# Kernel tuning notes

Hardware: AMD Instinct MI355X
Metric: run time of the kernel (lower is better)

The kernel has to match this reference:

```python
import jax, jax.numpy as jnp
import numpy as np

NUM_EMB = 16384
EMB_DIM = 64
BETA = 0.25  # commitment_cost, legacy=True formulation


def _l2norm(x, axis=-1):
    # matches F.normalize(p=2): x / max(||x||, 1e-12)
    n = jnp.sqrt(jnp.sum(x * x, axis=axis, keepdims=True))
    return x / jnp.maximum(n, 1e-12)


def setup_inputs() -> dict:
    key = jax.random.key(0)
    k_z, k_cb, k_w, k_b = jax.random.split(key, 4)
    z = jax.random.normal(k_z, (16, 1024, EMB_DIM), dtype=jnp.float32)
    # frozen codebook: N(0, d^{-0.5})
    codebook = jax.random.normal(k_cb, (NUM_EMB, EMB_DIM), dtype=jnp.float32) * (EMB_DIM ** -0.5)
    # Linear(d, d) default init: U(-1/sqrt(d), 1/sqrt(d))
    lim = 1.0 / np.sqrt(EMB_DIM)
    proj_w = jax.random.uniform(k_w, (EMB_DIM, EMB_DIM), dtype=jnp.float32, minval=-lim, maxval=lim)
    proj_b = jax.random.uniform(k_b, (EMB_DIM,), dtype=jnp.float32, minval=-lim, maxval=lim)
    scale = jnp.float32(10.0)  # l2_norm_scale
    return {"z": z, "codebook": codebook, "proj_w": proj_w, "proj_b": proj_b, "scale": scale}


def reference(z, codebook, proj_w, proj_b, scale):
    B, T, d = z.shape
    zf = z.reshape(-1, d)                                   # [BT, d]
    quant_codebook = codebook @ proj_w.T + proj_b           # [N, d]
    zn = _l2norm(zf)
    cn = _l2norm(quant_codebook)
    distances = -jnp.einsum('bd,nd->bn', zn, cn) * scale    # [BT, N]
    idx = jnp.argmin(distances, axis=1)                     # [BT]
    quantized = quant_codebook[idx].reshape(z.shape)        # [B, T, d]
    sg = jax.lax.stop_gradient
    commitment_loss = jnp.mean((sg(quantized) - z) ** 2)
    codebook_loss = jnp.mean((quantized - sg(z)) ** 2)
    vq_loss = commitment_loss + BETA * codebook_loss        # legacy=True
    quantized_st = z + sg(quantized - z)                    # straight-through
    return quantized_st, vq_loss, idx.reshape(B, T)
```

## Files before the change

kernel.cpp:

```cpp
#include <hip/hip_runtime.h>
#include <hip/hip_bf16.h>


#define NCODES 16384
#define NTOK   16384
#define DIM    64
#define MARGIN_MFMA 8e-3f
#define CAP    16

typedef __attribute__((ext_vector_type(8))) short bf16x8;
typedef __attribute__((ext_vector_type(4))) float f32x4;
#define GLOBAL_AS __attribute__((address_space(1)))
#define LDS_AS    __attribute__((address_space(3)))

__device__ float  g_qcb[NCODES * DIM];
__device__ short  g_cnb[NCODES * DIM];
__device__ short  g_znb[NTOK * DIM];
__device__ unsigned g_topu[NTOK];
__device__ int    g_candcnt[NTOK];
__device__ int    g_cand[NTOK * CAP];
__device__ int    g_wl[NTOK];
__device__ int    g_wln;
__device__ float  g_partial[512];

__device__ __forceinline__ float wave_sum64(float v) {
#pragma unroll
  for (int o = 32; o > 0; o >>= 1) v += __shfl_xor(v, o, 64);
  return v;
}
__device__ __forceinline__ short f2bf(float f) {
  __hip_bfloat16 h = __float2bfloat16(f);
  return *reinterpret_cast<short*>(&h);
}
__device__ __forceinline__ float bf2f(short s) {
  __hip_bfloat16 h = *reinterpret_cast<__hip_bfloat16*>(&s);
  return __bfloat162float(h);
}
__device__ __forceinline__ void split8(const float* v, bf16x8& hi, bf16x8& lo) {
#pragma unroll
  for (int i = 0; i < 8; ++i) {
    float f = v[i];
    short h = f2bf(f);
    hi[i] = h;
    lo[i] = f2bf(f - bf2f(h));
  }
}

__global__ __launch_bounds__(256) void k_prep(const float* __restrict__ cb,
                                              const float* __restrict__ pw,
                                              const float* __restrict__ pb,
                                              const float* __restrict__ z) {
  int tid = threadIdx.x;
  int wave = tid >> 6, lane = tid & 63, quad = lane >> 4, col = lane & 15;
  if (blockIdx.x < 256) {
    int rowBase = blockIdx.x * 64 + wave * 16;
    const float* cr = cb + (size_t)(rowBase + col) * 64 + quad * 8;
    bf16x8 ah0, al0, ah1, al1;
    split8(cr, ah0, al0);
    split8(cr + 32, ah1, al1);
    float vals[4][4];
    float nr[4] = {0.f, 0.f, 0.f, 0.f};
    const f32x4 fz = {0.f, 0.f, 0.f, 0.f};
#pragma unroll
    for (int nt = 0; nt < 4; ++nt) {
      int j = col + 16 * nt;
      const float* wr = pw + (size_t)j * 64 + quad * 8;
      bf16x8 bh0, bl0, bh1, bl1;
      split8(wr, bh0, bl0);
      split8(wr + 32, bh1, bl1);
      f32x4 d = __builtin_amdgcn_mfma_f32_16x16x32_bf16(ah0, bh0, fz, 0, 0, 0);
      d = __builtin_amdgcn_mfma_f32_16x16x32_bf16(ah1, bh1, d, 0, 0, 0);
      d = __builtin_amdgcn_mfma_f32_16x16x32_bf16(ah0, bl0, d, 0, 0, 0);
      d = __builtin_amdgcn_mfma_f32_16x16x32_bf16(ah1, bl1, d, 0, 0, 0);
      d = __builtin_amdgcn_mfma_f32_16x16x32_bf16(al0, bh0, d, 0, 0, 0);
      d = __builtin_amdgcn_mfma_f32_16x16x32_bf16(al1, bh1, d, 0, 0, 0);
      float bj = pb[j];
#pragma unroll
      for (int r = 0; r < 4; ++r) {
        float v = d[r] + bj;
        vals[nt][r] = v;
        nr[r] = fmaf(v, v, nr[r]);
      }
    }
#pragma unroll
    for (int r = 0; r < 4; ++r) {
      float v = nr[r];
      v += __shfl_xor(v, 1, 64);
      v += __shfl_xor(v, 2, 64);
      v += __shfl_xor(v, 4, 64);
      v += __shfl_xor(v, 8, 64);
      nr[r] = 1.0f / fmaxf(sqrtf(v), 1e-12f);
    }
#pragma unroll
    for (int nt = 0; nt < 4; ++nt)
#pragma unroll
      for (int r = 0; r < 4; ++r) {
        int row = rowBase + quad * 4 + r;
        int j = col + 16 * nt;
        g_qcb[(size_t)row * 64 + j] = vals[nt][r];
        g_cnb[(size_t)row * 64 + j] = f2bf(vals[nt][r] * nr[r]);
      }
  } else {
    int zb = blockIdx.x - 256;
    int gid = zb * 256 + tid;
    if (gid < NTOK) { g_topu[gid] = 0u; g_candcnt[gid] = 0; }
    if (gid == 0) g_wln = 0;
    int base = zb * 64;
    for (int r = 0; r < 16; ++r) {
      int row = base + wave * 16 + r;
      float v = z[(size_t)row * 64 + lane];
      float tot = wave_sum64(v * v);
      g_znb[(size_t)row * 64 + lane] = f2bf(v / fmaxf(sqrtf(tot), 1e-12f));
    }
  }
}

__global__ __launch_bounds__(256) void k_mfma1() {
  __shared__ __align__(16) short smB[2][8192];
  int tid = threadIdx.x;
  int wave = tid >> 6, lane = tid & 63;
  int quad = lane >> 4, col = lane & 15;
  int tokGroup = blockIdx.x >> 4, split = blockIdx.x & 15;
  int tokBase = tokGroup * 256 + wave * 64;

  const short* za = g_znb + (size_t)(tokBase + col) * 64 + quad * 8;
  bf16x8 A0[4], A1[4];
#pragma unroll
  for (int f = 0; f < 4; ++f) {
    A0[f] = *(const bf16x8*)(za + f * 16 * 64);
    A1[f] = *(const bf16x8*)(za + f * 16 * 64 + 32);
  }
  float m[4][4];
#pragma unroll
  for (int f = 0; f < 4; ++f)
#pragma unroll
    for (int r = 0; r < 4; ++r) m[f][r] = -3.0e38f;

  const char* gsplit = (const char*)(g_cnb + (size_t)split * 1024 * 64);
  int x = col & 7;
  int s0off = ((quad ^ x) << 3);
  int s1off = (((4 | quad) ^ x) << 3);
  int goff[4];
#pragma unroll
  for (int i = 0; i < 4; ++i) {
    int cidx = wave * 256 + i * 64 + lane;
    int row = cidx >> 3, sw = cidx & 7;
    goff[i] = row * 128 + ((sw ^ (row & 7)) << 4);
  }

#pragma unroll
  for (int i = 0; i < 4; ++i)
    __builtin_amdgcn_global_load_lds((const GLOBAL_AS void*)(gsplit + goff[i]),
                                     (LDS_AS void*)(&smB[0][wave * 2048 + i * 512]), 16, 0, 0);
  __syncthreads();

  int p = 0;
  for (int s = 0; s < 8; ++s) {
    if (s < 7) {
      const char* gb = gsplit + (size_t)(s + 1) * 16384;
#pragma unroll
      for (int i = 0; i < 4; ++i)
        __builtin_amdgcn_global_load_lds((const GLOBAL_AS void*)(gb + goff[i]),
                                         (LDS_AS void*)(&smB[p ^ 1][wave * 2048 + i * 512]),
                                         16, 0, 0);
    }
    const short* bufp = smB[p];
#pragma unroll
    for (int h = 0; h < 2; ++h) {
      bf16x8 B0[4], B1[4];
#pragma unroll
      for (int t = 0; t < 4; ++t) {
        const short* lb = bufp + ((h * 4 + t) * 16 + col) * 64;
        B0[t] = *(const bf16x8*)(lb + s0off);
        B1[t] = *(const bf16x8*)(lb + s1off);
      }
#pragma unroll
      for (int t = 0; t < 4; ++t) {
#pragma unroll
        for (int f = 0; f < 4; ++f) {
          f32x4 acc = {0.f, 0.f, 0.f, 0.f};
          acc = __builtin_amdgcn_mfma_f32_16x16x32_bf16(A0[f], B0[t], acc, 0, 0, 0);
          acc = __builtin_amdgcn_mfma_f32_16x16x32_bf16(A1[f], B1[t], acc, 0, 0, 0);
#pragma unroll
          for (int r = 0; r < 4; ++r) m[f][r] = fmaxf(m[f][r], acc[r]);
        }
      }
    }
    __syncthreads();
    p ^= 1;
  }

#pragma unroll
  for (int f = 0; f < 4; ++f)
#pragma unroll
    for (int r = 0; r < 4; ++r) {
      float v = m[f][r];
      v = fmaxf(v, __shfl_xor(v, 1, 64));
      v = fmaxf(v, __shfl_xor(v, 2, 64));
      v = fmaxf(v, __shfl_xor(v, 4, 64));
      v = fmaxf(v, __shfl_xor(v, 8, 64));
      if (col == 0) {
        unsigned b = __float_as_uint(v);
        unsigned e = (b & 0x80000000u) ? ~b : (b | 0x80000000u);
        atomicMax(&g_topu[tokBase + f * 16 + quad * 4 + r], e);
      }
    }
}

__global__ __launch_bounds__(256) void k_mfma2() {
  __shared__ __align__(16) short smB[2][8192];
  int tid = threadIdx.x;
  int wave = tid >> 6, lane = tid & 63;
  int quad = lane >> 4, col = lane & 15;
  int tokGroup = blockIdx.x >> 4, split = blockIdx.x & 15;
  int tokBase = tokGroup * 256 + wave * 64;

  const short* za = g_znb + (size_t)(tokBase + col) * 64 + quad * 8;
  bf16x8 A0[4], A1[4];
#pragma unroll
  for (int f = 0; f < 4; ++f) {
    A0[f] = *(const bf16x8*)(za + f * 16 * 64);
    A1[f] = *(const bf16x8*)(za + f * 16 * 64 + 32);
  }
  float th[4][4];
#pragma unroll
  for (int f = 0; f < 4; ++f)
#pragma unroll
    for (int r = 0; r < 4; ++r) {
      unsigned u = g_topu[tokBase + f * 16 + quad * 4 + r];
      unsigned b = (u & 0x80000000u) ? (u & 0x7FFFFFFFu) : ~u;
      th[f][r] = __uint_as_float(b) - MARGIN_MFMA;
    }

  const char* gsplit = (const char*)(g_cnb + (size_t)split * 1024 * 64);
  int x = col & 7;
  int s0off = ((quad ^ x) << 3);
  int s1off = (((4 | quad) ^ x) << 3);
  int goff[4];
#pragma unroll
  for (int i = 0; i < 4; ++i) {
    int cidx = wave * 256 + i * 64 + lane;
    int row = cidx >> 3, sw = cidx & 7;
    goff[i] = row * 128 + ((sw ^ (row & 7)) << 4);
  }

#pragma unroll
  for (int i = 0; i < 4; ++i)
    __builtin_amdgcn_global_load_lds((const GLOBAL_AS void*)(gsplit + goff[i]),
                                     (LDS_AS void*)(&smB[0][wave * 2048 + i * 512]), 16, 0, 0);
  __syncthreads();

  int codeB = split * 1024 + col;
  int p = 0;
  for (int s = 0; s < 8; ++s) {
    if (s < 7) {
      const char* gb = gsplit + (size_t)(s + 1) * 16384;
#pragma unroll
      for (int i = 0; i < 4; ++i)
        __builtin_amdgcn_global_load_lds((const GLOBAL_AS void*)(gb + goff[i]),
                                         (LDS_AS void*)(&smB[p ^ 1][wave * 2048 + i * 512]),
                                         16, 0, 0);
    }
    const short* bufp = smB[p];
#pragma unroll
    for (int h = 0; h < 2; ++h) {
      bf16x8 B0[4], B1[4];
#pragma unroll
      for (int t = 0; t < 4; ++t) {
        const short* lb = bufp + ((h * 4 + t) * 16 + col) * 64;
        B0[t] = *(const bf16x8*)(lb + s0off);
        B1[t] = *(const bf16x8*)(lb + s1off);
      }
#pragma unroll
      for (int t = 0; t < 4; ++t) {
        int code = codeB + s * 128 + (h * 4 + t) * 16;
#pragma unroll
        for (int f = 0; f < 4; ++f) {
          f32x4 acc = {0.f, 0.f, 0.f, 0.f};
          acc = __builtin_amdgcn_mfma_f32_16x16x32_bf16(A0[f], B0[t], acc, 0, 0, 0);
          acc = __builtin_amdgcn_mfma_f32_16x16x32_bf16(A1[f], B1[t], acc, 0, 0, 0);
          float dmax = fmaxf(fmaxf(acc[0] - th[f][0], acc[1] - th[f][1]),
                             fmaxf(acc[2] - th[f][2], acc[3] - th[f][3]));
          if (dmax >= 0.f) {
#pragma unroll
            for (int r = 0; r < 4; ++r) {
              if (acc[r] >= th[f][r]) {
                int tok = tokBase + f * 16 + quad * 4 + r;
                int pos = atomicAdd(&g_candcnt[tok], 1);
                if (pos < CAP) g_cand[tok * CAP + pos] = code;
              }
            }
          }
        }
      }
    }
    __syncthreads();
    p ^= 1;
  }
}

__global__ __launch_bounds__(256) void k_scan() {
  __shared__ int flags[256];
  __shared__ int sbase;
  int tid = threadIdx.x;
  int tok = blockIdx.x * 256 + tid;
  int flag = (g_candcnt[tok] >= 2) ? 1 : 0;
  flags[tid] = flag;
  __syncthreads();
  if (tid == 0) {
    int run = 0;
    for (int i = 0; i < 256; ++i) {
      int f = flags[i];
      flags[i] = run;
      run += f;
    }
    sbase = atomicAdd(&g_wln, run);
  }
  __syncthreads();
  if (flag) g_wl[sbase + flags[tid]] = tok;
}

__global__ __launch_bounds__(256) void k_arb(const float* __restrict__ z,
                                             const float* __restrict__ cb,
                                             const float* __restrict__ pw,
                                             const float* __restrict__ pb) {
  __shared__ double WT[64 * 65];
  __shared__ float cbl[4][64];
  int tid = threadIdx.x;
  int wave = tid >> 6, lane = tid & 63;
  for (int e = tid; e < 4096; e += 256) {
    int j = e >> 6, k = e & 63;
    WT[k * 65 + j] = (double)pw[e];
  }
  __syncthreads();

  int wln = g_wln;
  double bj = (double)pb[lane];
  int gwave = blockIdx.x * 4 + wave;

  for (int e = gwave; e < wln; e += 4096) {
    int tok = g_wl[e];
    int cnt = g_candcnt[tok];
    double zj = (double)z[(size_t)tok * 64 + lane];
    double best = -1.0e300;
    int bi = 0x7FFFFFFF;
    int lim = (cnt <= CAP) ? cnt : 0;
    for (int c = 0; c < lim; ++c) {
      int code = g_cand[tok * CAP + c];
      cbl[wave][lane] = cb[(size_t)code * 64 + lane];
      double s0 = 0.0, s1 = 0.0, s2 = 0.0, s3 = 0.0;
#pragma unroll
      for (int kk = 0; kk < 16; ++kk) {
        s0 = fma(WT[kk * 65 + lane], (double)cbl[wave][kk], s0);
        s1 = fma(WT[(kk + 16) * 65 + lane], (double)cbl[wave][kk + 16], s1);
        s2 = fma(WT[(kk + 32) * 65 + lane], (double)cbl[wave][kk + 32], s2);
        s3 = fma(WT[(kk + 48) * 65 + lane], (double)cbl[wave][kk + 48], s3);
      }
      double qc = ((s0 + s1) + (s2 + s3)) + bj;
      double s = zj * qc, n2 = qc * qc;
#pragma unroll
      for (int o = 32; o > 0; o >>= 1) {
        s += __shfl_xor(s, o, 64);
        n2 += __shfl_xor(n2, o, 64);
      }
      double key = s / fmax(sqrt(n2), 1e-12);
      if (key > best || (key == best && code < bi)) { best = key; bi = code; }
    }
    if (cnt > CAP) {
      for (int code = 0; code < NCODES; ++code) {
        cbl[wave][lane] = cb[(size_t)code * 64 + lane];
        double s0 = 0.0, s1 = 0.0, s2 = 0.0, s3 = 0.0;
#pragma unroll
        for (int kk = 0; kk < 16; ++kk) {
          s0 = fma(WT[kk * 65 + lane], (double)cbl[wave][kk], s0);
          s1 = fma(WT[(kk + 16) * 65 + lane], (double)cbl[wave][kk + 16], s1);
          s2 = fma(WT[(kk + 32) * 65 + lane], (double)cbl[wave][kk + 32], s2);
          s3 = fma(WT[(kk + 48) * 65 + lane], (double)cbl[wave][kk + 48], s3);
        }
        double qc = ((s0 + s1) + (s2 + s3)) + bj;
        double s = zj * qc, n2 = qc * qc;
#pragma unroll
        for (int o = 32; o > 0; o >>= 1) {
          s += __shfl_xor(s, o, 64);
          n2 += __shfl_xor(n2, o, 64);
        }
        double key = s / fmax(sqrt(n2), 1e-12);
        if (key > best || (key == best && code < bi)) { best = key; bi = code; }
      }
    }
    if (lane == 0) g_cand[tok * CAP] = bi;
  }
}

__global__ __launch_bounds__(256) void k_out(const float* __restrict__ z,
                                             float* __restrict__ out0,
                                             float* __restrict__ out2) {
  __shared__ float ws[4];
  int tid = threadIdx.x;
  int wave = tid >> 6, lane = tid & 63;
  int base = blockIdx.x * 32;
  float lsum = 0.f;
  for (int r = 0; r < 8; ++r) {
    int tok = base + wave * 8 + r;
    int idx = g_cand[tok * CAP];
    float q = g_qcb[(size_t)idx * 64 + lane];
    float zv = z[(size_t)tok * 64 + lane];
    float d = q - zv;
    out0[(size_t)tok * 64 + lane] = zv + d;
    lsum = fmaf(d, d, lsum);
    if (lane == 0) out2[tok] = (float)idx;
  }
  float tot = wave_sum64(lsum);
  if (lane == 0) ws[wave] = tot;
  __syncthreads();
  if (tid == 0) g_partial[blockIdx.x] = ((ws[0] + ws[1]) + (ws[2] + ws[3]));
}

__global__ void k_loss(float* __restrict__ out1) {
  int lane = threadIdx.x;
  float s = 0.f;
#pragma unroll
  for (int i = 0; i < 8; ++i) s += g_partial[lane + 64 * i];
  s = wave_sum64(s);
  if (lane == 0) out1[0] = 1.25f * s / 1048576.0f;
}

extern "C" void kernel_launch(void* const* d_in, const int* in_sizes, int n_in,
                              void* d_out, int out_size, void* d_ws, size_t ws_size,
                              hipStream_t stream) {
  const float* z = (const float*)d_in[0];
  const float* cb = (const float*)d_in[1];
  const float* pw = (const float*)d_in[2];
  const float* pb = (const float*)d_in[3];

  float* out0 = (float*)d_out;
  float* out1 = out0 + (size_t)NTOK * DIM;
  float* out2 = out1 + 1;

  hipLaunchKernelGGL(k_prep, dim3(512), dim3(256), 0, stream, cb, pw, pb, z);
  hipLaunchKernelGGL(k_mfma1, dim3(1024), dim3(256), 0, stream);
  hipLaunchKernelGGL(k_mfma2, dim3(1024), dim3(256), 0, stream);
  hipLaunchKernelGGL(k_scan, dim3(64), dim3(256), 0, stream);
  hipLaunchKernelGGL(k_arb, dim3(1024), dim3(256), 0, stream, z, cb, pw, pb);
  hipLaunchKernelGGL(k_out, dim3(512), dim3(256), 0, stream, z, out0, out2);
  hipLaunchKernelGGL(k_loss, dim3(1), dim3(64), 0, stream, out1);
}
```

Baseline: 194.2 us.

## Fuse scan, arbitration, output and loss kernels into one final kernel

Replaces the worklist scan, the fp64 arbitration kernel, the output kernel and the single-block loss kernel with one kernel. Each wave arbitrates its own ambiguous tokens in place and then writes the outputs. The loss is reduced by the last block to finish, found through an atomic counter with release/acquire ordering. This removes three launches and the worklist round trip. The cost is that arbitration work is no longer load-balanced across waves and each block must stage the fp64 weight matrix in LDS, with only 512 blocks instead of 1024.

```diff
diff --git a/kernel.cpp b/kernel.cpp
--- a/kernel.cpp
+++ b/kernel.cpp
@@ -19,8 +19,7 @@
 __device__ unsigned g_topu[NTOK];
 __device__ int    g_candcnt[NTOK];
 __device__ int    g_cand[NTOK * CAP];
-__device__ int    g_wl[NTOK];
-__device__ int    g_wln;
+__device__ int    g_done;
 __device__ float  g_partial[512];
 
 __device__ __forceinline__ float wave_sum64(float v) {
@@ -104,7 +103,7 @@
     int zb = blockIdx.x - 256;
     int gid = zb * 256 + tid;
     if (gid < NTOK) { g_topu[gid] = 0u; g_candcnt[gid] = 0; }
-    if (gid == 0) g_wln = 0;
+    if (gid == 0) g_done = 0;
     int base = zb * 64;
     for (int r = 0; r < 16; ++r) {
       int row = base + wave * 16 + r;
@@ -299,33 +298,17 @@
   }
 }
 
-__global__ __launch_bounds__(256) void k_scan() {
-  __shared__ int flags[256];
-  __shared__ int sbase;
-  int tid = threadIdx.x;
-  int tok = blockIdx.x * 256 + tid;
-  int flag = (g_candcnt[tok] >= 2) ? 1 : 0;
-  flags[tid] = flag;
-  __syncthreads();
-  if (tid == 0) {
-    int run = 0;
-    for (int i = 0; i < 256; ++i) {
-      int f = flags[i];
-      flags[i] = run;
-      run += f;
-    }
-    sbase = atomicAdd(&g_wln, run);
-  }
-  __syncthreads();
-  if (flag) g_wl[sbase + flags[tid]] = tok;
-}
-
-__global__ __launch_bounds__(256) void k_arb(const float* __restrict__ z,
-                                             const float* __restrict__ cb,
-                                             const float* __restrict__ pw,
-                                             const float* __restrict__ pb) {
+__global__ __launch_bounds__(256) void k_final(const float* __restrict__ z,
+                                               const float* __restrict__ cb,
+                                               const float* __restrict__ pw,
+                                               const float* __restrict__ pb,
+                                               float* __restrict__ out0,
+                                               float* __restrict__ out1,
+                                               float* __restrict__ out2) {
   __shared__ double WT[64 * 65];
   __shared__ float cbl[4][64];
+  __shared__ float ws[4];
+  __shared__ int lastFlag;
   int tid = threadIdx.x;
   int wave = tid >> 6, lane = tid & 63;
   for (int e = tid; e < 4096; e += 256) {
@@ -334,40 +317,20 @@
   }
   __syncthreads();
 
-  int wln = g_wln;
   double bj = (double)pb[lane];
-  int gwave = blockIdx.x * 4 + wave;
-
-  for (int e = gwave; e < wln; e += 4096) {
-    int tok = g_wl[e];
+  int base = blockIdx.x * 32;
+  float lsum = 0.f;
+  for (int r8 = 0; r8 < 8; ++r8) {
+    int tok = base + wave * 8 + r8;
     int cnt = g_candcnt[tok];
-    double zj = (double)z[(size_t)tok * 64 + lane];
-    double best = -1.0e300;
-    int bi = 0x7FFFFFFF;
-    int lim = (cnt <= CAP) ? cnt : 0;
-    for (int c = 0; c < lim; ++c) {
-      int code = g_cand[tok * CAP + c];
-      cbl[wave][lane] = cb[(size_t)code * 64 + lane];
-      double s0 = 0.0, s1 = 0.0, s2 = 0.0, s3 = 0.0;
-#pragma unroll
-      for (int kk = 0; kk < 16; ++kk) {
-        s0 = fma(WT[kk * 65 + lane], (double)cbl[wave][kk], s0);
-        s1 = fma(WT[(kk + 16) * 65 + lane], (double)cbl[wave][kk + 16], s1);
-        s2 = fma(WT[(kk + 32) * 65 + lane], (double)cbl[wave][kk + 32], s2);
-        s3 = fma(WT[(kk + 48) * 65 + lane], (double)cbl[wave][kk + 48], s3);
-      }
-      double qc = ((s0 + s1) + (s2 + s3)) + bj;
-      double s = zj * qc, n2 = qc * qc;
-#pragma unroll
-      for (int o = 32; o > 0; o >>= 1) {
-        s += __shfl_xor(s, o, 64);
-        n2 += __shfl_xor(n2, o, 64);
-      }
-      double key = s / fmax(sqrt(n2), 1e-12);
-      if (key > best || (key == best && code < bi)) { best = key; bi = code; }
-    }
-    if (cnt > CAP) {
-      for (int code = 0; code < NCODES; ++code) {
+    int idx = g_cand[tok * CAP];
+    if (cnt >= 2) {
+      double zj = (double)z[(size_t)tok * 64 + lane];
+      double best = -1.0e300;
+      int bi = 0x7FFFFFFF;
+      int lim = (cnt <= CAP) ? cnt : 0;
+      for (int c = 0; c < lim; ++c) {
+        int code = g_cand[tok * CAP + c];
         cbl[wave][lane] = cb[(size_t)code * 64 + lane];
         double s0 = 0.0, s1 = 0.0, s2 = 0.0, s3 = 0.0;
 #pragma unroll
@@ -387,22 +350,30 @@
         double key = s / fmax(sqrt(n2), 1e-12);
         if (key > best || (key == best && code < bi)) { best = key; bi = code; }
       }
-    }
-    if (lane == 0) g_cand[tok * CAP] = bi;
-  }
-}
-
-__global__ __launch_bounds__(256) void k_out(const float* __restrict__ z,
-                                             float* __restrict__ out0,
-                                             float* __restrict__ out2) {
-  __shared__ float ws[4];
-  int tid = threadIdx.x;
-  int wave = tid >> 6, lane = tid & 63;
-  int base = blockIdx.x * 32;
-  float lsum = 0.f;
-  for (int r = 0; r < 8; ++r) {
-    int tok = base + wave * 8 + r;
-    int idx = g_cand[tok * CAP];
+      if (cnt > CAP) {
+        for (int code = 0; code < NCODES; ++code) {
+          cbl[wave][lane] = cb[(size_t)code * 64 + lane];
+          double s0 = 0.0, s1 = 0.0, s2 = 0.0, s3 = 0.0;
+#pragma unroll
+          for (int kk = 0; kk < 16; ++kk) {
+            s0 = fma(WT[kk * 65 + lane], (double)cbl[wave][kk], s0);
+            s1 = fma(WT[(kk + 16) * 65 + lane], (double)cbl[wave][kk + 16], s1);
+            s2 = fma(WT[(kk + 32) * 65 + lane], (double)cbl[wave][kk + 32], s2);
+            s3 = fma(WT[(kk + 48) * 65 + lane], (double)cbl[wave][kk + 48], s3);
+          }
+          double qc = ((s0 + s1) + (s2 + s3)) + bj;
+          double s = zj * qc, n2 = qc * qc;
+#pragma unroll
+          for (int o = 32; o > 0; o >>= 1) {
+            s += __shfl_xor(s, o, 64);
+            n2 += __shfl_xor(n2, o, 64);
+          }
+          double key = s / fmax(sqrt(n2), 1e-12);
+          if (key > best || (key == best && code < bi)) { best = key; bi = code; }
+        }
+      }
+      idx = bi;
+    }
     float q = g_qcb[(size_t)idx * 64 + lane];
     float zv = z[(size_t)tok * 64 + lane];
     float d = q - zv;
@@ -413,16 +384,24 @@
   float tot = wave_sum64(lsum);
   if (lane == 0) ws[wave] = tot;
   __syncthreads();
-  if (tid == 0) g_partial[blockIdx.x] = ((ws[0] + ws[1]) + (ws[2] + ws[3]));
-}
-
-__global__ void k_loss(float* __restrict__ out1) {
-  int lane = threadIdx.x;
-  float s = 0.f;
-#pragma unroll
-  for (int i = 0; i < 8; ++i) s += g_partial[lane + 64 * i];
-  s = wave_sum64(s);
-  if (lane == 0) out1[0] = 1.25f * s / 1048576.0f;
+  if (tid == 0) {
+    float p = ((ws[0] + ws[1]) + (ws[2] + ws[3]));
+    __hip_atomic_store(&g_partial[blockIdx.x], p, __ATOMIC_RELEASE,
+                       __HIP_MEMORY_SCOPE_AGENT);
+    int prev = __hip_atomic_fetch_add(&g_done, 1, __ATOMIC_ACQ_REL,
+                                      __HIP_MEMORY_SCOPE_AGENT);
+    lastFlag = (prev == 511) ? 1 : 0;
+  }
+  __syncthreads();
+  if (lastFlag && wave == 0) {
+    float s = 0.f;
+#pragma unroll
+    for (int i = 0; i < 8; ++i)
+      s += __hip_atomic_load(&g_partial[lane + 64 * i], __ATOMIC_ACQUIRE,
+                             __HIP_MEMORY_SCOPE_AGENT);
+    s = wave_sum64(s);
+    if (lane == 0) out1[0] = 1.25f * s / 1048576.0f;
+  }
 }
 
 extern "C" void kernel_launch(void* const* d_in, const int* in_sizes, int n_in,
@@ -440,8 +419,6 @@
   hipLaunchKernelGGL(k_prep, dim3(512), dim3(256), 0, stream, cb, pw, pb, z);
   hipLaunchKernelGGL(k_mfma1, dim3(1024), dim3(256), 0, stream);
   hipLaunchKernelGGL(k_mfma2, dim3(1024), dim3(256), 0, stream);
-  hipLaunchKernelGGL(k_scan, dim3(64), dim3(256), 0, stream);
-  hipLaunchKernelGGL(k_arb, dim3(1024), dim3(256), 0, stream, z, cb, pw, pb);
-  hipLaunchKernelGGL(k_out, dim3(512), dim3(256), 0, stream, z, out0, out2);
-  hipLaunchKernelGGL(k_loss, dim3(1), dim3(64), 0, stream, out1);
-}
+  hipLaunchKernelGGL(k_final, dim3(512), dim3(256), 0, stream, z, cb, pw, pb,
+                     out0, out1, out2);
+}
```

Measured after the change: 202.6 us. +4.3%, slower.
